# Performance work log

Hardware: AMD Instinct MI355X
Metric: run time of the kernel (lower is better)

Reference implementation:

```python
import jax, jax.numpy as jnp
import numpy as np

B, S, D, H = 2, 2048, 1024, 16


def setup_inputs() -> dict:
    key = jax.random.key(0)
    kq, kk, kv, kw = jax.random.split(key, 4)
    Q = jax.random.normal(kq, (B, S, D), dtype=jnp.float32)
    K = jax.random.normal(kk, (B, S, D), dtype=jnp.float32)
    V = jax.random.normal(kv, (B, S, D), dtype=jnp.float32)
    Wo = jax.random.normal(kw, (D, D), dtype=jnp.float32) * (1.0 / np.sqrt(D))
    return {"Q": Q, "K": K, "V": V, "Wo": Wo, "num_heads": H}


def reference(Q, K, V, Wo, num_heads):
    b, s, d = Q.shape
    dk = d // num_heads
    # split heads: [B,S,D] -> [B,H,S,dk]
    q = Q.reshape(b, s, num_heads, dk).transpose(0, 2, 1, 3)
    k = K.reshape(b, s, num_heads, dk).transpose(0, 2, 1, 3)
    v = V.reshape(b, s, num_heads, dk).transpose(0, 2, 1, 3)
    scale = 1.0 / jnp.sqrt(jnp.asarray(dk, dtype=q.dtype))
    logits = jnp.einsum('bhqd,bhkd->bhqk', q, k) * scale  # [B,H,S,S]
    probs = jax.nn.softmax(logits, axis=-1).astype(q.dtype)
    o = jnp.einsum('bhqk,bhkd->bhqd', probs, v)  # [B,H,S,dk]
    o = o.transpose(0, 2, 1, 3).reshape(b, s, d)  # concat heads
    # O = einsum('d dkh, ... dkh -> ... d', Wo, scores) == scores @ Wo^T
    return jnp.einsum('dk,bsk->bsd', Wo, o)
```

## Files before the change

kernel.cpp:

```cpp
#include <hip/hip_runtime.h>
#include <hip/hip_bf16.h>

#define B_ 2
#define S_ 2048
#define D_ 1024
#define H_ 16
#define DK_ 64

typedef __hip_bfloat16 bf16;
typedef short v8s __attribute__((ext_vector_type(8)));
typedef short v4s __attribute__((ext_vector_type(4)));
typedef float v4f __attribute__((ext_vector_type(4)));
typedef float v16f __attribute__((ext_vector_type(16)));
typedef int   v4i __attribute__((ext_vector_type(4)));
typedef int   v2i __attribute__((ext_vector_type(2)));

static __device__ __forceinline__ v16f mfma32(v8s a, v8s b, v16f c) {
  return __builtin_amdgcn_mfma_f32_32x32x16_bf16(a, b, c, 0, 0, 0);
}
static __device__ __forceinline__ void gl2lds16(const void* g, void* l) {
  __builtin_amdgcn_global_load_lds((const __attribute__((address_space(1))) void*)g,
                                   (__attribute__((address_space(3))) void*)l,
                                   16, 0, 0);
}
static __device__ __forceinline__ short f2bf(float x) {
  return (short)__builtin_bit_cast(unsigned short, __float2bfloat16(x));
}
static __device__ __forceinline__ int pk2f(float lo, float hi) {
  unsigned a = __builtin_bit_cast(unsigned, lo) + 0x8000u;
  unsigned b = __builtin_bit_cast(unsigned, hi) + 0x8000u;
  return (int)__builtin_amdgcn_perm(b, a, 0x07060302u);
}
static __device__ __forceinline__ float bf2f(short s) {
  return __builtin_bit_cast(float, ((unsigned)(unsigned short)s) << 16);
}

__global__ __launch_bounds__(256) void pre_kernel(
    const float* __restrict__ K, const float* __restrict__ V,
    const float* __restrict__ Wo, bf16* __restrict__ Kb,
    bf16* __restrict__ Vt, bf16* __restrict__ Wb)
{
  __shared__ __align__(16) bf16 td[64 * 72];
  const int t = threadIdx.x;
  const int bx = blockIdx.x;

  if (bx < 2048) {
    const int idx = bx * 256 + t;
    const int seg = idx & 7;
    const int rest = idx >> 3;
    const int h = rest & 15;
    const int bs = rest >> 4;
    const float* src = K + (size_t)bs * D_ + h * 64 + seg * 8;
    v4f x = *(const v4f*)src, y = *(const v4f*)(src + 4);
    v8s r;
    r[0]=f2bf(x[0]); r[1]=f2bf(x[1]); r[2]=f2bf(x[2]); r[3]=f2bf(x[3]);
    r[4]=f2bf(y[0]); r[5]=f2bf(y[1]); r[6]=f2bf(y[2]); r[7]=f2bf(y[3]);
    const int b = bs >> 11, s = bs & 2047;
    *(v8s*)(Kb + ((size_t)(b * H_ + h) * S_ + s) * DK_ + seg * 8) = r;
  } else if (bx < 3072) {
    const int idx = bx - 2048;
    const int bh = idx >> 5, b = bh >> 4, h = bh & 15;
    const int s0 = (idx & 31) * 64;
    const int srow = t >> 2;
    const int cs = t & 3;
    const float* vp = V + (size_t)(b * S_ + s0 + srow) * D_ + h * 64 + cs * 16;
#pragma unroll
    for (int j = 0; j < 4; j++) {
      v4f x = *(const v4f*)(vp + j * 4);
#pragma unroll
      for (int jj = 0; jj < 4; jj++)
        td[(cs * 16 + j * 4 + jj) * 72 + srow] = __float2bfloat16(x[jj]);
    }
    __syncthreads();
    const int d = t >> 2;
#pragma unroll
    for (int a2 = 0; a2 < 4; a2++) {
      const int pos = cs * 16 + a2 * 4;
      const int g = pos >> 5;
      const int a = (pos >> 2) & 7;
      const int kbase = g * 32 + ((a >> 2) << 4) + ((a & 1) << 3) + (((a >> 1) & 1) << 2);
      v4s val = *(const v4s*)(td + d * 72 + kbase);
      *(v4s*)(Vt + ((size_t)bh * DK_ + d) * S_ + s0 + pos) = val;
    }
  } else {
    const int i = ((bx - 3072) * 256 + t) * 4;
    v4f a = *(const v4f*)(Wo + i);
    v4s r;
    r[0]=f2bf(a[0]); r[1]=f2bf(a[1]); r[2]=f2bf(a[2]); r[3]=f2bf(a[3]);
    *(v4s*)((short*)Wb + i) = r;
  }
}

__global__ __launch_bounds__(256, 4) void attn4_kernel(
    const float* __restrict__ Q, const bf16* __restrict__ Kb,
    const bf16* __restrict__ Vt, bf16* __restrict__ Op0,
    bf16* __restrict__ Op1, float* __restrict__ Lp)
{
  __shared__ __align__(16) bf16 kk[2][64 * 64];
  __shared__ __align__(16) bf16 vv[2][64 * 64];

  const int t = threadIdx.x;
  const int w = t >> 6, l = t & 63, h2 = l >> 5, ln = l & 31;
  const int bh = blockIdx.x, b = bh >> 4, h = bh & 15;
  const int qbase = blockIdx.y * 128 + w * 32;
  const int z = blockIdx.z;
  const int kb0 = z << 10;

  const bf16* Kbh = Kb + (size_t)bh * (S_ * DK_);
  const bf16* Vbh = Vt + (size_t)bh * (DK_ * S_);

  const float sc = 0.18033688011112042f;
  v8s bq[4];
  {
    const float* qp = Q + ((size_t)b * S_ + qbase + ln) * D_ + h * DK_ + h2 * 8;
#pragma unroll
    for (int c = 0; c < 4; c++) {
      v4f x = *(const v4f*)(qp + c * 16);
      v4f y = *(const v4f*)(qp + c * 16 + 4);
      v4i r = { pk2f(x[0]*sc, x[1]*sc), pk2f(x[2]*sc, x[3]*sc),
                pk2f(y[0]*sc, y[1]*sc), pk2f(y[2]*sc, y[3]*sc) };
      bq[c] = __builtin_bit_cast(v8s, r);
    }
  }

  v16f Z;
#pragma unroll
  for (int r = 0; r < 16; r++) Z[r] = 0.f;

  v16f accA, accB;
#pragma unroll
  for (int r = 0; r < 16; r++) { accA[r] = 0.f; accB[r] = 0.f; }
  float lpart = 0.f;

#pragma unroll
  for (int j = 0; j < 2; j++) {
    const int flat = j * 256 + t, row = flat >> 3, sp = flat & 7;
    gl2lds16(Kbh + (size_t)(kb0 + row) * DK_ + ((sp ^ (row & 7)) * 8), &kk[0][flat * 8]);
    gl2lds16(Vbh + (size_t)row * S_ + kb0 + ((sp ^ (row & 7)) * 8), &vv[0][flat * 8]);
  }

  int it = 0;
  for (int kb = kb0; kb < kb0 + 1024; kb += 64, it ^= 1) {
    __syncthreads();
    if (kb + 64 < kb0 + 1024) {
#pragma unroll
      for (int j = 0; j < 2; j++) {
        const int flat = j * 256 + t, row = flat >> 3, sp = flat & 7;
        gl2lds16(Kbh + (size_t)(kb + 64 + row) * DK_ + ((sp ^ (row & 7)) * 8),
                 &kk[it ^ 1][flat * 8]);
        gl2lds16(Vbh + (size_t)row * S_ + (kb + 64) + ((sp ^ (row & 7)) * 8),
                 &vv[it ^ 1][flat * 8]);
      }
    }
    const bf16* kc_ = kk[it];
    const bf16* vc_ = vv[it];

    v16f s0, s1;
#pragma unroll
    for (int c = 0; c < 4; c++) {
      const int sd = 2 * c + h2;
      v8s a0 = *(const v8s*)(kc_ + ln * 64 + ((sd ^ (ln & 7)) * 8));
      v8s a1 = *(const v8s*)(kc_ + (32 + ln) * 64 + ((sd ^ (ln & 7)) * 8));
      if (c == 0) {
        s0 = mfma32(a0, bq[0], Z);
        s1 = mfma32(a1, bq[0], Z);
      } else {
        s0 = mfma32(a0, bq[c], s0);
        s1 = mfma32(a1, bq[c], s1);
      }
    }

    float p0[16], p1[16];
#pragma unroll
    for (int r = 0; r < 16; r++) { p0[r] = exp2f(s0[r]); p1[r] = exp2f(s1[r]); }
    float suA = 0.f, suB = 0.f;
#pragma unroll
    for (int r = 0; r < 16; r++) { suA += p0[r]; suB += p1[r]; }
    lpart += suA + suB;

    v4i i00 = { pk2f(p0[0],p0[1]),  pk2f(p0[2],p0[3]),  pk2f(p0[4],p0[5]),  pk2f(p0[6],p0[7]) };
    v4i i01 = { pk2f(p0[8],p0[9]),  pk2f(p0[10],p0[11]),pk2f(p0[12],p0[13]),pk2f(p0[14],p0[15]) };
    v4i i10 = { pk2f(p1[0],p1[1]),  pk2f(p1[2],p1[3]),  pk2f(p1[4],p1[5]),  pk2f(p1[6],p1[7]) };
    v4i i11 = { pk2f(p1[8],p1[9]),  pk2f(p1[10],p1[11]),pk2f(p1[12],p1[13]),pk2f(p1[14],p1[15]) };
    v8s pb00 = __builtin_bit_cast(v8s, i00);
    v8s pb01 = __builtin_bit_cast(v8s, i01);
    v8s pb10 = __builtin_bit_cast(v8s, i10);
    v8s pb11 = __builtin_bit_cast(v8s, i11);

#pragma unroll
    for (int st = 0; st < 2; st++) {
#pragma unroll
      for (int kc = 0; kc < 2; kc++) {
        const int q = st * 4 + kc * 2 + h2;
        v8s avA = *(const v8s*)(vc_ + ln * 64 + ((q ^ (ln & 7)) * 8));
        v8s avB = *(const v8s*)(vc_ + (32 + ln) * 64 + ((q ^ (ln & 7)) * 8));
        v8s pb = st ? (kc ? pb11 : pb10) : (kc ? pb01 : pb00);
        accA = mfma32(avA, pb, accA);
        accB = mfma32(avB, pb, accB);
      }
    }
  }

  __syncthreads();
  const float lfull = lpart + __shfl_xor(lpart, 32);
  bf16* epw = &kk[0][0] + w * 2048;
#pragma unroll
  for (int r = 0; r < 16; r += 4) {
    const int off = 4 * h2;
    const int sgA = (r >> 2) ^ (ln & 3);
    const int sgB = 4 + sgA;
    v2i pa = { pk2f(accA[r],   accA[r+1]),
               pk2f(accA[r+2], accA[r+3]) };
    v2i pb = { pk2f(accB[r],   accB[r+1]),
               pk2f(accB[r+2], accB[r+3]) };
    *(v2i*)(epw + ln * 64 + sgA * 8 + off) = pa;
    *(v2i*)(epw + ln * 64 + sgB * 8 + off) = pb;
  }
  if (h2 == 0)
    Lp[((size_t)z * 32 + bh) * S_ + qbase + ln] = lfull;

  bf16* Op = z ? Op1 : Op0;
#pragma unroll
  for (int i = 0; i < 4; i++) {
    const int flat = i * 64 + l;
    const int qr = flat >> 3, sd = flat & 7;
    const int phys = ((sd & 3) ^ (qr & 3)) | (sd & 4);
    v8s val = *(const v8s*)(epw - w * 2048 + (w * 32 + qr) * 64 + phys * 8);
    *(v8s*)(Op + ((size_t)b * S_ + qbase - w * 32 + w * 32 + qr) * D_ + h * DK_ + sd * 8) = val;
  }
}

__global__ __launch_bounds__(256, 4) void projm_kernel(
    const bf16* __restrict__ Op0, const bf16* __restrict__ Op1,
    const float* __restrict__ Lp, const bf16* __restrict__ Wo,
    float* __restrict__ Out)
{
  __shared__ __align__(16) bf16 aa[2][64 * 64];
  __shared__ __align__(16) bf16 bb[2][64 * 64];

  const int t = threadIdx.x;
  const int w = t >> 6, l = t & 63, h2 = l >> 5, ln = l & 31;
  const int m0 = blockIdx.x * 64, n0 = blockIdx.y * 64;
  const int wm = (w & 1) * 32, wn = (w >> 1) * 32;
  const int b = m0 >> 11;

  v16f acc;
#pragma unroll
  for (int r = 0; r < 16; r++) acc[r] = 0.f;

  auto stage_load = [&](int k0, int j, v8s& a, v8s& c, float& inv) {
    const int flat = j * 256 + t, row = flat >> 3, sp = flat & 7;
    const int m = m0 + row, s = m & 2047;
    const int h = k0 >> 6;
    const size_t off = (size_t)m * D_ + k0 + ((sp ^ (row & 7)) * 8);
    a = *(const v8s*)(Op0 + off);
    c = *(const v8s*)(Op1 + off);
    const float l0 = Lp[(size_t)(b * H_ + h) * S_ + s];
    const float l1 = Lp[(size_t)(32 + b * H_ + h) * S_ + s];
    inv = 1.0f / (l0 + l1);
  };
  auto stage_write = [&](int buf, int j, v8s a, v8s c, float inv) {
    const int flat = j * 256 + t;
    v4i A = __builtin_bit_cast(v4i, a), C = __builtin_bit_cast(v4i, c);
    v4i r;
#pragma unroll
    for (int jj = 0; jj < 4; jj++) {
      const unsigned aw = (unsigned)A[jj], cw = (unsigned)C[jj];
      const float alo = __builtin_bit_cast(float, aw << 16);
      const float ahi = __builtin_bit_cast(float, aw & 0xffff0000u);
      const float clo = __builtin_bit_cast(float, cw << 16);
      const float chi = __builtin_bit_cast(float, cw & 0xffff0000u);
      r[jj] = pk2f((alo + clo) * inv, (ahi + chi) * inv);
    }
    *(v4i*)(&aa[buf][flat * 8]) = r;
  };

  v8s a0v, c0v, a1v, c1v; float i0v, i1v;
  stage_load(0, 0, a0v, c0v, i0v);
  stage_load(0, 1, a1v, c1v, i1v);
#pragma unroll
  for (int j = 0; j < 2; j++) {
    const int flat = j * 256 + t, row = flat >> 3, sp = flat & 7;
    gl2lds16(Wo + (size_t)(n0 + row) * D_ + ((sp ^ (row & 7)) * 8), &bb[0][flat * 8]);
  }
  stage_write(0, 0, a0v, c0v, i0v);
  stage_write(0, 1, a1v, c1v, i1v);

  int it = 0;
  for (int k0 = 0; k0 < D_; k0 += 64, it ^= 1) {
    __syncthreads();
    const bool nxt = (k0 + 64 < D_);
    if (nxt) {
      stage_load(k0 + 64, 0, a0v, c0v, i0v);
      stage_load(k0 + 64, 1, a1v, c1v, i1v);
#pragma unroll
      for (int j = 0; j < 2; j++) {
        const int flat = j * 256 + t, row = flat >> 3, sp = flat & 7;
        gl2lds16(Wo + (size_t)(n0 + row) * D_ + (k0 + 64) + ((sp ^ (row & 7)) * 8),
                 &bb[it ^ 1][flat * 8]);
      }
    }
    const bf16* ac = aa[it];
    const bf16* bc = bb[it];
#pragma unroll
    for (int c = 0; c < 4; c++) {
      const int sd = 2 * c + h2;
      v8s av = *(const v8s*)(ac + (wm + ln) * 64 + ((sd ^ (ln & 7)) * 8));
      v8s bv = *(const v8s*)(bc + (wn + ln) * 64 + ((sd ^ (ln & 7)) * 8));
      acc = mfma32(av, bv, acc);
    }
    if (nxt) {
      stage_write(it ^ 1, 0, a0v, c0v, i0v);
      stage_write(it ^ 1, 1, a1v, c1v, i1v);
    }
  }

#pragma unroll
  for (int r = 0; r < 16; r++) {
    const int row = m0 + wm + (r & 3) + 4 * h2 + 8 * (r >> 2);
    Out[(size_t)row * D_ + n0 + wn + ln] = acc[r];
  }
}

extern "C" void kernel_launch(void* const* d_in, const int* in_sizes, int n_in,
                              void* d_out, int out_size, void* d_ws, size_t ws_size,
                              hipStream_t stream) {
  (void)in_sizes; (void)n_in; (void)out_size; (void)ws_size;
  const float* Q  = (const float*)d_in[0];
  const float* K  = (const float*)d_in[1];
  const float* V  = (const float*)d_in[2];
  const float* Wo = (const float*)d_in[3];
  float* out = (float*)d_out;

  bf16* base = (bf16*)d_ws;
  bf16* kb   = base;
  bf16* vt   = base + (size_t)4  * 1024 * 1024;
  bf16* wo_b = base + (size_t)8  * 1024 * 1024;
  bf16* op0  = base + (size_t)9  * 1024 * 1024;
  bf16* op1  = base + (size_t)13 * 1024 * 1024;
  float* lp  = (float*)(base + (size_t)17 * 1024 * 1024);

  pre_kernel  <<<dim3(4096),       256, 0, stream>>>(K, V, Wo, kb, vt, wo_b);
  attn4_kernel<<<dim3(32, 16, 2),  256, 0, stream>>>(Q, kb, vt, op0, op1, lp);
  projm_kernel<<<dim3(64, 16),     256, 0, stream>>>(op0, op1, lp, wo_b, out);
}
```

Baseline: 178.8 us.

## Load V directly from global into registers instead of staging through LDS

Drops the double-buffered LDS staging of the transposed V tile. Each lane now reads its V fragments straight from global memory, issued right after the QK MFMAs so they overlap with the exp2 work, and the MFMA blocks are wrapped with s_setprio to favour matrix issue. This halves LDS use and the LDS traffic per block, which may raise occupancy. In exchange, every one of the four waves repeats the same global V reads, and the load latency is exposed inside the loop.

```diff
diff --git a/kernel.cpp b/kernel.cpp
--- a/kernel.cpp
+++ b/kernel.cpp
@@ -97,7 +97,6 @@
     bf16* __restrict__ Op1, float* __restrict__ Lp)
 {
   __shared__ __align__(16) bf16 kk[2][64 * 64];
-  __shared__ __align__(16) bf16 vv[2][64 * 64];
 
   const int t = threadIdx.x;
   const int w = t >> 6, l = t & 63, h2 = l >> 5, ln = l & 31;
@@ -108,6 +107,8 @@
 
   const bf16* Kbh = Kb + (size_t)bh * (S_ * DK_);
   const bf16* Vbh = Vt + (size_t)bh * (DK_ * S_);
+  const bf16* vAp = Vbh + (size_t)ln * S_ + 8 * h2;
+  const bf16* vBp = Vbh + (size_t)(32 + ln) * S_ + 8 * h2;
 
   const float sc = 0.18033688011112042f;
   v8s bq[4];
@@ -136,7 +137,6 @@
   for (int j = 0; j < 2; j++) {
     const int flat = j * 256 + t, row = flat >> 3, sp = flat & 7;
     gl2lds16(Kbh + (size_t)(kb0 + row) * DK_ + ((sp ^ (row & 7)) * 8), &kk[0][flat * 8]);
-    gl2lds16(Vbh + (size_t)row * S_ + kb0 + ((sp ^ (row & 7)) * 8), &vv[0][flat * 8]);
   }
 
   int it = 0;
@@ -148,14 +148,12 @@
         const int flat = j * 256 + t, row = flat >> 3, sp = flat & 7;
         gl2lds16(Kbh + (size_t)(kb + 64 + row) * DK_ + ((sp ^ (row & 7)) * 8),
                  &kk[it ^ 1][flat * 8]);
-        gl2lds16(Vbh + (size_t)row * S_ + (kb + 64) + ((sp ^ (row & 7)) * 8),
-                 &vv[it ^ 1][flat * 8]);
       }
     }
     const bf16* kc_ = kk[it];
-    const bf16* vc_ = vv[it];
 
     v16f s0, s1;
+    __builtin_amdgcn_s_setprio(1);
 #pragma unroll
     for (int c = 0; c < 4; c++) {
       const int sd = 2 * c + h2;
@@ -169,6 +167,16 @@
         s1 = mfma32(a1, bq[c], s1);
       }
     }
+    __builtin_amdgcn_s_setprio(0);
+
+    v8s vA0 = *(const v8s*)(vAp + kb);
+    v8s vA1 = *(const v8s*)(vAp + kb + 16);
+    v8s vA2 = *(const v8s*)(vAp + kb + 32);
+    v8s vA3 = *(const v8s*)(vAp + kb + 48);
+    v8s vB0 = *(const v8s*)(vBp + kb);
+    v8s vB1 = *(const v8s*)(vBp + kb + 16);
+    v8s vB2 = *(const v8s*)(vBp + kb + 32);
+    v8s vB3 = *(const v8s*)(vBp + kb + 48);
 
     float p0[16], p1[16];
 #pragma unroll
@@ -187,18 +195,16 @@
     v8s pb10 = __builtin_bit_cast(v8s, i10);
     v8s pb11 = __builtin_bit_cast(v8s, i11);
 
-#pragma unroll
-    for (int st = 0; st < 2; st++) {
-#pragma unroll
-      for (int kc = 0; kc < 2; kc++) {
-        const int q = st * 4 + kc * 2 + h2;
-        v8s avA = *(const v8s*)(vc_ + ln * 64 + ((q ^ (ln & 7)) * 8));
-        v8s avB = *(const v8s*)(vc_ + (32 + ln) * 64 + ((q ^ (ln & 7)) * 8));
-        v8s pb = st ? (kc ? pb11 : pb10) : (kc ? pb01 : pb00);
-        accA = mfma32(avA, pb, accA);
-        accB = mfma32(avB, pb, accB);
-      }
-    }
+    __builtin_amdgcn_s_setprio(1);
+    accA = mfma32(vA0, pb00, accA);
+    accB = mfma32(vB0, pb00, accB);
+    accA = mfma32(vA1, pb01, accA);
+    accB = mfma32(vB1, pb01, accB);
+    accA = mfma32(vA2, pb10, accA);
+    accB = mfma32(vB2, pb10, accB);
+    accA = mfma32(vA3, pb11, accA);
+    accB = mfma32(vB3, pb11, accB);
+    __builtin_amdgcn_s_setprio(0);
   }
 
   __syncthreads();
```

Result: slower. 216.2 us (+20.9%).
